# Optimization experiments

Measured on AMD Instinct MI355X. Metric: run time of the kernel, lower is better.

Reference implementation:

```python
import jax, jax.numpy as jnp
import numpy as np
from math import sqrt

P_DROP = 0.2  # dropout_rate

def setup_inputs() -> dict:
    key = jax.random.key(0)
    ks = jax.random.split(key, 5)
    B, Cin, H, W = 32, 128, 64, 64
    Cout, kh, kw = 256, 3, 3
    k = sqrt(1.0 / (Cin * kh * kw))  # He-style init std from module
    x = jax.random.normal(ks[0], (B, Cin, H, W), dtype=jnp.float32)
    weight = jax.random.normal(ks[1], (Cout, Cin, kh, kw), dtype=jnp.float32) * k
    bias = jax.random.normal(ks[2], (Cout,), dtype=jnp.float32) * k
    # uniforms used for torch.rand(...) > p per batch element ('w' mode draws fresh masks per sample)
    u_w = jax.random.uniform(ks[3], (B, Cout, Cin, kh, kw), dtype=jnp.float32)
    u_b = jax.random.uniform(ks[4], (B, Cout), dtype=jnp.float32)
    return {"x": x, "weight": weight, "bias": bias, "u_w": u_w, "u_b": u_b}

def reference(x, weight, bias, u_w, u_b):
    # 'w' mode: per-sample dropped-out weight/bias, conv per sample -> vmapped batched conv.
    # Note: mask is (rand > p) with NO 1/(1-p) rescaling, matching the torch code.
    w_mask = (u_w > P_DROP).astype(weight.dtype)          # [B,O,I,kh,kw]
    b_mask = (u_b > P_DROP).astype(bias.dtype)            # [B,O]
    w_per = weight[None] * w_mask                          # [B,O,I,kh,kw]
    b_per = bias[None] * b_mask                            # [B,O]

    def conv_one(xi, wi):  # xi: [Cin,H,W], wi: [O,I,kh,kw]
        return jax.lax.conv_general_dilated(
            xi[None], wi,
            window_strides=(1, 1),
            padding=((1, 1), (1, 1)),
            dimension_numbers=("NCHW", "OIHW", "NCHW"),
        )[0]

    y = jax.vmap(conv_one)(x, w_per)                       # [B,O,H,W]
    return y + b_per[:, :, None, None]
```

## Files before the change

kernel.cpp:

```cpp
#include <hip/hip_runtime.h>
#include <cstdint>
#include <cstddef>

#define CIN   128
#define COUT  256
#define HW    64
#define NSP   4096
#define KTOT  1152
#define BATCH 32
#define PDROP 0.2f
#define LDT   40

__device__ __forceinline__ unsigned short f2bf(float f) {
    unsigned int u = __builtin_bit_cast(unsigned int, f);
    u += 0x7fffu + ((u >> 16) & 1u);
    return (unsigned short)(u >> 16);
}

__device__ __align__(16) unsigned short g_zeros[64] = {0};

__device__ __forceinline__ void gl_lds16(const unsigned short* g, unsigned short* l) {
    __builtin_amdgcn_global_load_lds(
        (const __attribute__((address_space(1))) unsigned int*)g,
        (__attribute__((address_space(3))) unsigned int*)l,
        16, 0, 0);
}

__global__ __launch_bounds__(256) void prepass(
        const float* __restrict__ weight, const float* __restrict__ u_w,
        const float* __restrict__ x,
        unsigned short* __restrict__ wt, unsigned short* __restrict__ xt)
{
    __shared__ unsigned short sh[8704];
    const int t256 = threadIdx.x;

    if (blockIdx.x < 4096) {
        const int half = t256 >> 7;
        const int t    = t256 & 127;
        const int bo   = blockIdx.x * 2 + half;
        const int o    = bo & (COUT - 1);
        unsigned short* tile = sh + half * KTOT;
        const float4* wsrc = reinterpret_cast<const float4*>(weight + (size_t)o  * KTOT);
        const float4* usrc = reinterpret_cast<const float4*>(u_w    + (size_t)bo * KTOT);
        #pragma unroll
        for (int j = 0; j < 3; ++j) {
            const int idx = j * 128 + t;
            if (idx < KTOT / 4) {
                float4 wv = wsrc[idx];
                float4 uv = usrc[idx];
                const float w4[4] = {wv.x, wv.y, wv.z, wv.w};
                const float u4[4] = {uv.x, uv.y, uv.z, uv.w};
                #pragma unroll
                for (int c = 0; c < 4; ++c) {
                    const int ks = idx * 4 + c;
                    const int i  = ks / 9;
                    const int r  = ks - 9 * i;
                    tile[r * CIN + i] = f2bf((u4[c] > PDROP) ? w4[c] : 0.f);
                }
            }
        }
        __syncthreads();
        const uint4* src = reinterpret_cast<const uint4*>(tile);
        uint4* dst = reinterpret_cast<uint4*>(wt + (size_t)bo * KTOT);
        #pragma unroll
        for (int j = 0; j < 2; ++j) {
            const int idx = j * 128 + t;
            if (idx < KTOT / 8) dst[idx] = src[idx];
        }
    } else {
        const int bidx = blockIdx.x - 4096;
        const int b    = bidx >> 6;
        const int hw0  = (bidx & 63) * 64;
        const int ib   = t256 >> 4;
        const int hw4  = (t256 & 15) * 4;
        #pragma unroll
        for (int j = 0; j < 8; ++j) {
            const int i = ib + 16 * j;
            const float4 v = *reinterpret_cast<const float4*>(
                x + ((size_t)(b * CIN + i)) * NSP + hw0 + hw4);
            const float v4[4] = {v.x, v.y, v.z, v.w};
            #pragma unroll
            for (int c = 0; c < 4; ++c)
                sh[(hw4 + c) * 136 + i] = f2bf(v4[c]);
        }
        __syncthreads();
        #pragma unroll
        for (int j = 0; j < 4; ++j) {
            const int idx  = j * 256 + t256;
            const int row  = idx >> 4;
            const int part = idx & 15;
            const uint4 v = *reinterpret_cast<const uint4*>(&sh[row * 136 + part * 8]);
            *reinterpret_cast<uint4*>(
                xt + ((size_t)(b * NSP + hw0 + row)) * CIN + part * 8) = v;
        }
    }
}

__global__ __launch_bounds__(256, 3) void conv_v4(
        const unsigned short* __restrict__ wt,
        const unsigned short* __restrict__ xt,
        const float* __restrict__ bias, const float* __restrict__ u_b,
        float* __restrict__ out)
{
    using frag  = __attribute__((ext_vector_type(8))) short;
    using f32x4 = __attribute__((ext_vector_type(4))) float;

    __shared__ unsigned short Xs[4 * 66 * 64];
    __shared__ unsigned short As[128 * 64];

    const int tid  = threadIdx.x;
    const int lane = tid & 63;
    const int q    = lane >> 4;
    const int l15  = lane & 15;
    const int wv   = tid >> 6;
    const int wm   = (wv >> 1) * 64;
    const int wn   = (wv & 1) * 64;
    const int wnrow = wn >> 6;

    const int b   = blockIdx.z;
    const int m0  = blockIdx.y * 128;
    const int n0  = blockIdx.x * 128;
    const int ph0 = n0 >> 6;

    const unsigned short* wtb = wt + (size_t)(b * COUT + m0) * KTOT;
    const unsigned short* xtb = xt + (size_t)b * NSP * CIN;

    const int r8 = lane >> 3;
    const int p8 = lane & 7;
    const int cx = p8 ^ r8;
    const unsigned short* gA[4];
    unsigned short* ldsA[4];
    #pragma unroll
    for (int j = 0; j < 4; ++j) {
        const int row = wv * 32 + j * 8 + r8;
        gA[j]   = wtb + (size_t)row * KTOT + cx * 8;
        ldsA[j] = &As[(wv * 32 + j * 8) * 64];
    }

    const int kcl = (lane & 7) ^ ((1 + (lane >> 3)) & 7);
    const int xsrc_lane = (lane >> 3) * CIN + kcl * 8;
    const int hhx = ph0 - 1 + wv;
    const bool vrow = ((unsigned)hhx < 64u);
    unsigned short* const xdst = &Xs[(wv * 66 + 1) * 64];

    const int l7 = l15 & 7;
    const int physk0 = q ^ l7;
    const int physk1 = (4 + q) ^ l7;
    const int a_base = (wm + l15) * 64;
    int xoff[4];
    #pragma unroll
    for (int ni = 0; ni < 4; ++ni) xoff[ni] = (ni * 16 + l15 + 1) * 64;
    int xr[3][2];
    #pragma unroll
    for (int dxi = 0; dxi < 3; ++dxi)
        #pragma unroll
        for (int ki = 0; ki < 2; ++ki)
            xr[dxi][ki] = ((ki * 4 + q) ^ ((l15 + dxi) & 7)) * 8;

    f32x4 acc[4][4];
    #pragma unroll
    for (int i = 0; i < 4; ++i)
        #pragma unroll
        for (int j = 0; j < 4; ++j)
            acc[i][j] = (f32x4){0.f, 0.f, 0.f, 0.f};

    {
        const int cell = tid >> 5;
        const int rr   = cell >> 1;
        const int cc   = (cell & 1) ? 65 : 0;
        *reinterpret_cast<unsigned int*>(
            &Xs[(rr * 66 + cc) * 64 + (tid & 31) * 2]) = 0u;
    }

    #pragma unroll
    for (int s2 = 0; s2 < 2; ++s2) {
        const int i0 = s2 * 64;

        __syncthreads();

        {
            const unsigned short* sx = vrow
                ? xtb + (size_t)hhx * HW * CIN + i0 + xsrc_lane
                : g_zeros;
            #pragma unroll
            for (int g = 0; g < 8; ++g)
                gl_lds16(vrow ? (sx + g * 8 * CIN) : sx, xdst + g * 512);
        }

        #pragma unroll
        for (int tap = 0; tap < 9; ++tap) {
            const int dy  = tap / 3 - 1;
            const int dx  = tap - 3 * (tap / 3) - 1;
            const int dxi = dx + 1;

            if (tap) __syncthreads();

            const int k0 = tap * 128 + i0;
            #pragma unroll
            for (int j = 0; j < 4; ++j)
                gl_lds16(gA[j] + k0, ldsA[j]);

            __syncthreads();

            const int cb = (wnrow + dy + 1) * 4224 + dx * 64;

            #pragma unroll
            for (int ki = 0; ki < 2; ++ki) {
                const int pk = ki ? physk1 : physk0;
                frag af[4], bfr[4];
                #pragma unroll
                for (int mi = 0; mi < 4; ++mi)
                    af[mi] = *reinterpret_cast<const frag*>(
                        &As[a_base + mi * 1024 + pk * 8]);
                #pragma unroll
                for (int ni = 0; ni < 4; ++ni)
                    bfr[ni] = *reinterpret_cast<const frag*>(
                        &Xs[cb + xoff[ni] + xr[dxi][ki]]);
                #pragma unroll
                for (int mi = 0; mi < 4; ++mi)
                    #pragma unroll
                    for (int ni = 0; ni < 4; ++ni)
                        acc[mi][ni] = __builtin_amdgcn_mfma_f32_16x16x32_bf16(
                            af[mi], bfr[ni], acc[mi][ni], 0, 0, 0);
            }
        }
    }

    float* ob = out + (size_t)b * COUT * NSP;
    #pragma unroll
    for (int mi = 0; mi < 4; ++mi) {
        #pragma unroll
        for (int rg = 0; rg < 4; ++rg) {
            const int o  = m0 + wm + mi * 16 + q * 4 + rg;
            const float bvv = (u_b[b * COUT + o] > PDROP) ? bias[o] : 0.f;
            float* orow = ob + (size_t)o * NSP + n0 + wn + l15;
            #pragma unroll
            for (int ni = 0; ni < 4; ++ni)
                orow[ni * 16] = acc[mi][ni][rg] + bvv;
        }
    }
}

template<bool USE_WS>
__global__ __launch_bounds__(256) void conv_fb(
        const float* __restrict__ x, const float* __restrict__ weight,
        const float* __restrict__ bias, const float* __restrict__ u_w,
        const float* __restrict__ u_b, const unsigned short* __restrict__ wt,
        float* __restrict__ out)
{
    using frag  = __attribute__((ext_vector_type(8))) short;
    using f32x4 = __attribute__((ext_vector_type(4))) float;

    __shared__ unsigned short As[128 * LDT];
    __shared__ unsigned short Bs[128 * LDT];

    const int tid  = threadIdx.x;
    const int lane = tid & 63;
    const int q    = lane >> 4;
    const int l15  = lane & 15;
    const int wv   = tid >> 6;
    const int wm   = (wv >> 1) * 64;
    const int wn   = (wv & 1) * 64;

    const int b  = blockIdx.z;
    const int m0 = blockIdx.y * 128;
    const int n0 = blockIdx.x * 128;

    const int arow = tid >> 1;
    const int acol = (tid & 1) * 16;
    const int pn = tid & 127;
    const int kh = (tid >> 7) * 16;
    const int p  = n0 + pn;
    const int ph = p >> 6;
    const int pw = p & 63;

    const float* xb = x + (size_t)b * CIN * NSP;

    f32x4 acc[4][4];
    #pragma unroll
    for (int i = 0; i < 4; ++i)
        #pragma unroll
        for (int j = 0; j < 4; ++j)
            acc[i][j] = (f32x4){0.f, 0.f, 0.f, 0.f};

    const int a_rd = (wm + l15) * LDT + q * 8;
    const int b_rd = (wn + l15) * LDT + q * 8;

    for (int s = 0; s < 36; ++s) {
        const int r  = s >> 2;
        const int i0 = (s & 3) * 32;
        const int k0 = s * 32;

        uint4 av0, av1;
        float aw[16], au[16];
        if (USE_WS) {
            const uint4* src = reinterpret_cast<const uint4*>(
                wt + ((size_t)(b * COUT + m0 + arow)) * KTOT + k0 + acol);
            av0 = src[0];
            av1 = src[1];
        } else {
            const float* wsrc = weight + (size_t)(m0 + arow) * KTOT;
            const float* usrc = u_w + (size_t)(b * COUT + m0 + arow) * KTOT;
            #pragma unroll
            for (int ii = 0; ii < 16; ++ii) {
                const int kk = (i0 + acol + ii) * 9 + r;
                aw[ii] = wsrc[kk];
                au[ii] = usrc[kk];
            }
        }

        const int hh = ph + (r / 3) - 1;
        const int ww = pw + (r % 3) - 1;
        float bx[16];
        #pragma unroll
        for (int j = 0; j < 16; ++j) bx[j] = 0.f;
        if (((unsigned)hh < 64u) && ((unsigned)ww < 64u)) {
            const float* xsrc = xb + (size_t)(i0 + kh) * NSP + hh * HW + ww;
            #pragma unroll
            for (int j = 0; j < 16; ++j) bx[j] = xsrc[(size_t)j * NSP];
        }

        __syncthreads();

        if (USE_WS) {
            uint4* d = reinterpret_cast<uint4*>(&As[arow * LDT + acol]);
            d[0] = av0; d[1] = av1;
        } else {
            union { unsigned short u16[16]; uint4 v[2]; } tu;
            #pragma unroll
            for (int ii = 0; ii < 16; ++ii)
                tu.u16[ii] = f2bf((au[ii] > PDROP) ? aw[ii] : 0.f);
            uint4* d = reinterpret_cast<uint4*>(&As[arow * LDT + acol]);
            d[0] = tu.v[0]; d[1] = tu.v[1];
        }
        {
            union { unsigned short u16[16]; uint4 v[2]; } tu;
            #pragma unroll
            for (int j = 0; j < 16; ++j) tu.u16[j] = f2bf(bx[j]);
            uint4* d = reinterpret_cast<uint4*>(&Bs[pn * LDT + kh]);
            d[0] = tu.v[0]; d[1] = tu.v[1];
        }

        __syncthreads();

        frag af[4], bfr[4];
        #pragma unroll
        for (int mi = 0; mi < 4; ++mi)
            af[mi] = *reinterpret_cast<const frag*>(&As[a_rd + mi * 16 * LDT]);
        #pragma unroll
        for (int ni = 0; ni < 4; ++ni)
            bfr[ni] = *reinterpret_cast<const frag*>(&Bs[b_rd + ni * 16 * LDT]);
        #pragma unroll
        for (int mi = 0; mi < 4; ++mi)
            #pragma unroll
            for (int ni = 0; ni < 4; ++ni)
                acc[mi][ni] = __builtin_amdgcn_mfma_f32_16x16x32_bf16(
                    af[mi], bfr[ni], acc[mi][ni], 0, 0, 0);
    }

    float* ob = out + (size_t)b * COUT * NSP;
    #pragma unroll
    for (int mi = 0; mi < 4; ++mi) {
        #pragma unroll
        for (int rg = 0; rg < 4; ++rg) {
            const int o = m0 + wm + mi * 16 + q * 4 + rg;
            const float bvv = (u_b[b * COUT + o] > PDROP) ? bias[o] : 0.f;
            float* orow = ob + (size_t)o * NSP + n0 + wn + l15;
            #pragma unroll
            for (int ni = 0; ni < 4; ++ni)
                orow[ni * 16] = acc[mi][ni][rg] + bvv;
        }
    }
}

extern "C" void kernel_launch(void* const* d_in, const int* in_sizes, int n_in,
                              void* d_out, int out_size, void* d_ws, size_t ws_size,
                              hipStream_t stream)
{
    const float* x      = (const float*)d_in[0];
    const float* weight = (const float*)d_in[1];
    const float* bias   = (const float*)d_in[2];
    const float* u_w    = (const float*)d_in[3];
    const float* u_b    = (const float*)d_in[4];
    float* out = (float*)d_out;

    const size_t wt_bytes = (size_t)BATCH * COUT * KTOT * sizeof(unsigned short);
    const size_t xt_bytes = (size_t)BATCH * NSP * CIN * sizeof(unsigned short);
    dim3 grid(NSP / 128, COUT / 128, BATCH);

    if (ws_size >= wt_bytes + xt_bytes) {
        unsigned short* wtp = (unsigned short*)d_ws;
        unsigned short* xtp = (unsigned short*)((char*)d_ws + wt_bytes);
        prepass<<<4096 + 2048, 256, 0, stream>>>(weight, u_w, x, wtp, xtp);
        conv_v4<<<grid, 256, 0, stream>>>(wtp, xtp, bias, u_b, out);
    } else if (ws_size >= wt_bytes) {
        unsigned short* wtp = (unsigned short*)d_ws;
        prepass<<<4096, 256, 0, stream>>>(weight, u_w, x, wtp, nullptr);
        conv_fb<true><<<grid, 256, 0, stream>>>(x, weight, bias, u_w, u_b, wtp, out);
    } else {
        conv_fb<false><<<grid, 256, 0, stream>>>(x, weight, bias, u_w, u_b, nullptr, out);
    }
}
```

Measured before the change: 283.4 us.

## Double-buffer weight tiles in conv, remap block order, rework prepass transposes

Result: slower. 299.0 us (+5.5%).

```diff
diff --git a/kernel.cpp b/kernel.cpp
--- a/kernel.cpp
+++ b/kernel.cpp
@@ -31,42 +31,29 @@
         const float* __restrict__ x,
         unsigned short* __restrict__ wt, unsigned short* __restrict__ xt)
 {
-    __shared__ unsigned short sh[8704];
+    __shared__ unsigned int shp[64 * 65];
+    unsigned short* sh16 = reinterpret_cast<unsigned short*>(shp);
     const int t256 = threadIdx.x;
 
     if (blockIdx.x < 4096) {
         const int half = t256 >> 7;
-        const int t    = t256 & 127;
+        const int i    = t256 & 127;
         const int bo   = blockIdx.x * 2 + half;
         const int o    = bo & (COUT - 1);
-        unsigned short* tile = sh + half * KTOT;
-        const float4* wsrc = reinterpret_cast<const float4*>(weight + (size_t)o  * KTOT);
-        const float4* usrc = reinterpret_cast<const float4*>(u_w    + (size_t)bo * KTOT);
-        #pragma unroll
-        for (int j = 0; j < 3; ++j) {
-            const int idx = j * 128 + t;
-            if (idx < KTOT / 4) {
-                float4 wv = wsrc[idx];
-                float4 uv = usrc[idx];
-                const float w4[4] = {wv.x, wv.y, wv.z, wv.w};
-                const float u4[4] = {uv.x, uv.y, uv.z, uv.w};
-                #pragma unroll
-                for (int c = 0; c < 4; ++c) {
-                    const int ks = idx * 4 + c;
-                    const int i  = ks / 9;
-                    const int r  = ks - 9 * i;
-                    tile[r * CIN + i] = f2bf((u4[c] > PDROP) ? w4[c] : 0.f);
-                }
-            }
-        }
+        unsigned short* tile = sh16 + half * KTOT;
+        const float* wsrc = weight + (size_t)o  * KTOT + i * 9;
+        const float* usrc = u_w    + (size_t)bo * KTOT + i * 9;
+        float wv9[9], uv9[9];
+        #pragma unroll
+        for (int r = 0; r < 9; ++r) { wv9[r] = wsrc[r]; uv9[r] = usrc[r]; }
+        #pragma unroll
+        for (int r = 0; r < 9; ++r)
+            tile[r * CIN + i] = f2bf((uv9[r] > PDROP) ? wv9[r] : 0.f);
         __syncthreads();
         const uint4* src = reinterpret_cast<const uint4*>(tile);
         uint4* dst = reinterpret_cast<uint4*>(wt + (size_t)bo * KTOT);
-        #pragma unroll
-        for (int j = 0; j < 2; ++j) {
-            const int idx = j * 128 + t;
-            if (idx < KTOT / 8) dst[idx] = src[idx];
-        }
+        dst[i] = src[i];
+        if (i < 16) dst[128 + i] = src[128 + i];
     } else {
         const int bidx = blockIdx.x - 4096;
         const int b    = bidx >> 6;
@@ -74,14 +61,20 @@
         const int ib   = t256 >> 4;
         const int hw4  = (t256 & 15) * 4;
         #pragma unroll
-        for (int j = 0; j < 8; ++j) {
-            const int i = ib + 16 * j;
-            const float4 v = *reinterpret_cast<const float4*>(
-                x + ((size_t)(b * CIN + i)) * NSP + hw0 + hw4);
-            const float v4[4] = {v.x, v.y, v.z, v.w};
-            #pragma unroll
-            for (int c = 0; c < 4; ++c)
-                sh[(hw4 + c) * 136 + i] = f2bf(v4[c]);
+        for (int j = 0; j < 4; ++j) {
+            const int p = ib + 16 * j;
+            const float4 v0 = *reinterpret_cast<const float4*>(
+                x + ((size_t)(b * CIN + 2 * p)) * NSP + hw0 + hw4);
+            const float4 v1 = *reinterpret_cast<const float4*>(
+                x + ((size_t)(b * CIN + 2 * p + 1)) * NSP + hw0 + hw4);
+            const float e0[4] = {v0.x, v0.y, v0.z, v0.w};
+            const float e1[4] = {v1.x, v1.y, v1.z, v1.w};
+            #pragma unroll
+            for (int c = 0; c < 4; ++c) {
+                const unsigned int val =
+                    (unsigned int)f2bf(e0[c]) | ((unsigned int)f2bf(e1[c]) << 16);
+                shp[(hw4 + c) * 65 + p] = val;
+            }
         }
         __syncthreads();
         #pragma unroll
@@ -89,14 +82,18 @@
             const int idx  = j * 256 + t256;
             const int row  = idx >> 4;
             const int part = idx & 15;
-            const uint4 v = *reinterpret_cast<const uint4*>(&sh[row * 136 + part * 8]);
+            uint4 v;
+            v.x = shp[row * 65 + part * 4 + 0];
+            v.y = shp[row * 65 + part * 4 + 1];
+            v.z = shp[row * 65 + part * 4 + 2];
+            v.w = shp[row * 65 + part * 4 + 3];
             *reinterpret_cast<uint4*>(
                 xt + ((size_t)(b * NSP + hw0 + row)) * CIN + part * 8) = v;
         }
     }
 }
 
-__global__ __launch_bounds__(256, 3) void conv_v4(
+__global__ __launch_bounds__(256, 2) void conv_v5(
         const unsigned short* __restrict__ wt,
         const unsigned short* __restrict__ xt,
         const float* __restrict__ bias, const float* __restrict__ u_b,
@@ -106,7 +103,7 @@
     using f32x4 = __attribute__((ext_vector_type(4))) float;
 
     __shared__ unsigned short Xs[4 * 66 * 64];
-    __shared__ unsigned short As[128 * 64];
+    __shared__ unsigned short As[2][128 * 64];
 
     const int tid  = threadIdx.x;
     const int lane = tid & 63;
@@ -117,9 +114,11 @@
     const int wn   = (wv & 1) * 64;
     const int wnrow = wn >> 6;
 
-    const int b   = blockIdx.z;
-    const int m0  = blockIdx.y * 128;
-    const int n0  = blockIdx.x * 128;
+    const int f   = blockIdx.x + 32 * blockIdx.y + 64 * blockIdx.z;
+    const int wid = (f & 7) * 256 + (f >> 3);
+    const int b   = wid >> 6;
+    const int m0  = ((wid >> 5) & 1) * 128;
+    const int n0  = (wid & 31) * 128;
     const int ph0 = n0 >> 6;
 
     const unsigned short* wtb = wt + (size_t)(b * COUT + m0) * KTOT;
@@ -129,12 +128,10 @@
     const int p8 = lane & 7;
     const int cx = p8 ^ r8;
     const unsigned short* gA[4];
-    unsigned short* ldsA[4];
     #pragma unroll
     for (int j = 0; j < 4; ++j) {
         const int row = wv * 32 + j * 8 + r8;
-        gA[j]   = wtb + (size_t)row * KTOT + cx * 8;
-        ldsA[j] = &As[(wv * 32 + j * 8) * 64];
+        gA[j] = wtb + (size_t)row * KTOT + cx * 8;
     }
 
     const int kcl = (lane & 7) ^ ((1 + (lane >> 3)) & 7);
@@ -172,58 +169,68 @@
             &Xs[(rr * 66 + cc) * 64 + (tid & 31) * 2]) = 0u;
     }
 
-    #pragma unroll
-    for (int s2 = 0; s2 < 2; ++s2) {
-        const int i0 = s2 * 64;
-
-        __syncthreads();
-
-        {
-            const unsigned short* sx = vrow
-                ? xtb + (size_t)hhx * HW * CIN + i0 + xsrc_lane
-                : g_zeros;
-            #pragma unroll
-            for (int g = 0; g < 8; ++g)
-                gl_lds16(vrow ? (sx + g * 8 * CIN) : sx, xdst + g * 512);
-        }
-
-        #pragma unroll
-        for (int tap = 0; tap < 9; ++tap) {
-            const int dy  = tap / 3 - 1;
-            const int dx  = tap - 3 * (tap / 3) - 1;
-            const int dxi = dx + 1;
-
-            if (tap) __syncthreads();
-
-            const int k0 = tap * 128 + i0;
-            #pragma unroll
-            for (int j = 0; j < 4; ++j)
-                gl_lds16(gA[j] + k0, ldsA[j]);
-
-            __syncthreads();
-
-            const int cb = (wnrow + dy + 1) * 4224 + dx * 64;
-
-            #pragma unroll
-            for (int ki = 0; ki < 2; ++ki) {
-                const int pk = ki ? physk1 : physk0;
-                frag af[4], bfr[4];
-                #pragma unroll
-                for (int mi = 0; mi < 4; ++mi)
-                    af[mi] = *reinterpret_cast<const frag*>(
-                        &As[a_base + mi * 1024 + pk * 8]);
+    auto stage_a = [&](int k0, int buf) {
+        #pragma unroll
+        for (int j = 0; j < 4; ++j)
+            gl_lds16(gA[j] + k0, &As[buf][(wv * 32 + j * 8) * 64]);
+    };
+    auto stage_x = [&](int i0) {
+        const unsigned short* sx = vrow
+            ? xtb + (size_t)hhx * HW * CIN + i0 + xsrc_lane
+            : g_zeros;
+        #pragma unroll
+        for (int g = 0; g < 8; ++g)
+            gl_lds16(vrow ? (sx + g * 8 * CIN) : sx, xdst + g * 512);
+    };
+
+    stage_a(0, 0);
+    stage_x(0);
+
+    #pragma unroll
+    for (int it = 0; it < 18; ++it) {
+        const int tap = it % 9;
+        const int cur = it & 1;
+
+        if (it == 9) stage_x(64);
+
+        if (it < 17) {
+            const int nit = it + 1;
+            stage_a((nit % 9) * 128 + (nit / 9) * 64, nit & 1);
+        }
+
+        if (it == 0)      asm volatile("s_waitcnt vmcnt(4) lgkmcnt(0)" ::: "memory");
+        else if (it < 17) asm volatile("s_waitcnt vmcnt(4)" ::: "memory");
+        else              asm volatile("s_waitcnt vmcnt(0)" ::: "memory");
+        __builtin_amdgcn_s_barrier();
+
+        const int dy  = tap / 3 - 1;
+        const int dx  = tap - 3 * (tap / 3) - 1;
+        const int dxi = dx + 1;
+        const int cb  = (wnrow + dy + 1) * 4224 + dx * 64;
+
+        __builtin_amdgcn_s_setprio(1);
+        #pragma unroll
+        for (int ki = 0; ki < 2; ++ki) {
+            const int pk = ki ? physk1 : physk0;
+            frag af[4], bfr[4];
+            #pragma unroll
+            for (int mi = 0; mi < 4; ++mi)
+                af[mi] = *reinterpret_cast<const frag*>(
+                    &As[cur][a_base + mi * 1024 + pk * 8]);
+            #pragma unroll
+            for (int ni = 0; ni < 4; ++ni)
+                bfr[ni] = *reinterpret_cast<const frag*>(
+                    &Xs[cb + xoff[ni] + xr[dxi][ki]]);
+            #pragma unroll
+            for (int mi = 0; mi < 4; ++mi)
                 #pragma unroll
                 for (int ni = 0; ni < 4; ++ni)
-                    bfr[ni] = *reinterpret_cast<const frag*>(
-                        &Xs[cb + xoff[ni] + xr[dxi][ki]]);
-                #pragma unroll
-                for (int mi = 0; mi < 4; ++mi)
-                    #pragma unroll
-                    for (int ni = 0; ni < 4; ++ni)
-                        acc[mi][ni] = __builtin_amdgcn_mfma_f32_16x16x32_bf16(
-                            af[mi], bfr[ni], acc[mi][ni], 0, 0, 0);
-            }
-        }
+                    acc[mi][ni] = __builtin_amdgcn_mfma_f32_16x16x32_bf16(
+                        af[mi], bfr[ni], acc[mi][ni], 0, 0, 0);
+        }
+        __builtin_amdgcn_s_setprio(0);
+
+        if (it < 17) __builtin_amdgcn_s_barrier();
     }
 
     float* ob = out + (size_t)b * COUT * NSP;
@@ -392,7 +399,7 @@
         unsigned short* wtp = (unsigned short*)d_ws;
         unsigned short* xtp = (unsigned short*)((char*)d_ws + wt_bytes);
         prepass<<<4096 + 2048, 256, 0, stream>>>(weight, u_w, x, wtp, xtp);
-        conv_v4<<<grid, 256, 0, stream>>>(wtp, xtp, bias, u_b, out);
+        conv_v5<<<grid, 256, 0, stream>>>(wtp, xtp, bias, u_b, out);
     } else if (ws_size >= wt_bytes) {
         unsigned short* wtp = (unsigned short*)d_ws;
         prepass<<<4096, 256, 0, stream>>>(weight, u_w, x, wtp, nullptr);
```
